# Kernel optimization log

Measured on AMD Instinct MI355X. Metric: run time of the kernel, lower is better.

Reference implementation:

```python
import jax, jax.numpy as jnp
import numpy as np

NUM_HEADS = 8


def setup_inputs() -> dict:
    key = jax.random.key(0)
    ks = jax.random.split(key, 8)
    B, N, H, W = 8, 1024, 32, 32
    dim = H * W  # 1024
    x1 = jax.random.normal(ks[0], (B, N, H, W), dtype=jnp.float32)
    x2 = jax.random.normal(ks[1], (B, N, H, W), dtype=jnp.float32)
    conv_w = jax.random.normal(ks[2], (N, 2 * N, 3, 3), dtype=jnp.float32) * 0.01
    conv_b = jnp.zeros((N,), dtype=jnp.float32)
    wq = jax.random.normal(ks[3], (dim, dim), dtype=jnp.float32) * 0.02
    wk = jax.random.normal(ks[4], (dim, dim), dtype=jnp.float32) * 0.02
    wv = jax.random.normal(ks[5], (dim, dim), dtype=jnp.float32) * 0.02
    proj_w = jax.random.normal(ks[6], (dim, dim), dtype=jnp.float32) * 0.02
    proj_b = jnp.zeros((dim,), dtype=jnp.float32)
    return {"x1": x1, "x2": x2, "conv_w": conv_w, "conv_b": conv_b,
            "wq": wq, "wk": wk, "wv": wv, "proj_w": proj_w, "proj_b": proj_b}


def reference(x1, x2, conv_w, conv_b, wq, wk, wv, proj_w, proj_b):
    B, N, H, W = x1.shape
    C = H * W
    nh = NUM_HEADS
    hd = C // nh
    scale = hd ** -0.5

    # conv_cat: Conv2d(2N -> N, k=3, pad=1) on channel-concatenated inputs
    x_cat = jnp.concatenate([x1, x2], axis=1)  # [B, 2N, H, W]
    x_cat = jax.lax.conv_general_dilated(
        x_cat, conv_w, window_strides=(1, 1), padding=((1, 1), (1, 1)),
        dimension_numbers=("NCHW", "OIHW", "NCHW"))
    x_cat = x_cat + conv_b[None, :, None, None]
    x_cat = x_cat.reshape(B, N, C)  # [B, N, C]

    # torch Linear: y = x @ W.T (no bias, qkv_bias=False)
    def heads(t):  # [B, N, C] -> [B, nh, N, hd]
        return t.reshape(B, N, nh, hd).transpose(0, 2, 1, 3)

    q = heads(x1.reshape(B, N, C) @ wq.T)
    k = heads(x_cat @ wk.T)
    v = heads(x_cat @ wv.T)

    # attention: softmax(q k^T * scale) v   (dropout is identity at p=0)
    attn = jnp.einsum("bhnd,bhmd->bhnm", q, k) * scale
    attn = jax.nn.softmax(attn, axis=-1)
    x_attn = jnp.einsum("bhnm,bhmd->bhnd", attn, v)  # [B, nh, N, hd]
    x_attn = x_attn.transpose(0, 2, 1, 3).reshape(B, N, C)

    out = (x_attn @ proj_w.T + proj_b).reshape(B, N, H, W) + x1
    return out
```

## Files before the change

### kernel.cpp

```cpp
#include <hip/hip_runtime.h>
#include <hip/hip_bf16.h>
#include <cstdint>
#include <cstddef>

typedef __attribute__((ext_vector_type(8))) short short8;
typedef __attribute__((ext_vector_type(4))) float f32x4;
typedef unsigned short u16;

static __device__ __forceinline__ u16 f2bf(float f) {
  __hip_bfloat16 h = __float2bfloat16(f);
  return *reinterpret_cast<u16*>(&h);
}

static __device__ __forceinline__ void gload16(const void* g, void* l) {
  __builtin_amdgcn_global_load_lds(
      (const __attribute__((address_space(1))) void*)g,
      (__attribute__((address_space(3))) void*)l, 16, 0, 0);
}


__global__ void cast4_k(const float* __restrict__ a, const float* __restrict__ b,
                        const float* __restrict__ c, const float* __restrict__ d,
                        u16* __restrict__ oa, u16* __restrict__ ob,
                        u16* __restrict__ oc, u16* __restrict__ od) {
  const int which = blockIdx.y;
  const float* src = (which == 0) ? a : (which == 1) ? b : (which == 2) ? c : d;
  u16* dst = (which == 0) ? oa : (which == 1) ? ob : (which == 2) ? oc : od;
  int i = blockIdx.x * 256 + threadIdx.x;
  float4 v = ((const float4*)src)[i];
  union { u16 u[4]; uint2 p; } r;
  r.u[0] = f2bf(v.x); r.u[1] = f2bf(v.y); r.u[2] = f2bf(v.z); r.u[3] = f2bf(v.w);
  ((uint2*)dst)[i] = r.p;
}

__global__ void build_pad(const float* __restrict__ x1, const float* __restrict__ x2,
                          u16* __restrict__ in_t_pad, u16* __restrict__ x1b) {
  __shared__ float tile[64][65];
  const int it = blockIdx.x;
  const int st = blockIdx.y;
  const int b  = blockIdx.z;
  const int i0 = it * 64, s0 = st * 64;
  const bool isx1 = (i0 < 1024);
  const float* src = isx1
      ? x1 + ((size_t)b * 1024 + i0) * 1024
      : x2 + ((size_t)b * 1024 + (i0 - 1024)) * 1024;
  const int t = threadIdx.x;
  #pragma unroll
  for (int jj = 0; jj < 16; ++jj) {
    int idx = jj * 256 + t;
    int ii = idx >> 6, si = idx & 63;
    float v = src[(size_t)ii * 1024 + s0 + si];
    tile[ii][si] = v;
    if (isx1)
      x1b[((size_t)b * 1024 + i0 + ii) * 1024 + s0 + si] = f2bf(v);
  }
  __syncthreads();
  #pragma unroll
  for (int jj = 0; jj < 16; ++jj) {
    int idx = jj * 256 + t;
    int si = idx >> 6, ii = idx & 63;
    const int s = s0 + si;
    const int prow = (b * 34 + (s >> 5) + 1) * 34 + (s & 31) + 1;
    in_t_pad[(size_t)prow * 2048 + i0 + ii] = f2bf(tile[ii][si]);
  }
}

__global__ void pack_wp(const float* __restrict__ cw, u16* __restrict__ Wp) {
  __shared__ float sb[2304];
  const int blk = blockIdx.x;
  const int t = threadIdx.x;
  const size_t base = (size_t)blk * 2304;
  #pragma unroll
  for (int jj = 0; jj < 9; ++jj) sb[jj * 256 + t] = cw[base + jj * 256 + t];
  __syncthreads();
  const int p = blk * 256 + t;
  #pragma unroll
  for (int q = 0; q < 9; ++q)
    Wp[(size_t)q * 2097152 + p] = f2bf(sb[t * 9 + q]);
}

__global__ void addc_k(const float* __restrict__ p, const float* __restrict__ bias,
                       u16* __restrict__ xc) {
  __shared__ float tile[64][65];
  const int st = blockIdx.x;
  const int ot = blockIdx.y;
  const int b  = blockIdx.z;
  const int s0 = st * 64, o0 = ot * 64;
  const int t = threadIdx.x;
  const float* p1 = p + 8388608;
  #pragma unroll
  for (int jj = 0; jj < 16; ++jj) {
    int idx = jj * 256 + t;
    int si = idx >> 6, oi = idx & 63;
    const size_t m = ((size_t)b * 1024 + s0 + si) * 1024 + o0 + oi;
    tile[si][oi] = p[m] + p1[m] + bias[o0 + oi];
  }
  __syncthreads();
  #pragma unroll
  for (int jj = 0; jj < 16; ++jj) {
    int idx = jj * 256 + t;
    int oi = idx >> 6, si = idx & 63;
    xc[((size_t)b * 1024 + o0 + oi) * 1024 + s0 + si] = f2bf(tile[si][oi]);
  }
}

enum { GM_PLAIN = 0, GM_PROJ = 2 };

__global__ __launch_bounds__(256, 1)
void conv9_k(const u16* __restrict__ Ap, const u16* __restrict__ B,
             float* __restrict__ Cf) {
  __shared__ u16 lds[2 * 12288 + 3 * 8192];
  const int tid = threadIdx.x;
  const int lane = tid & 63, w = tid >> 6;
  const int l15 = lane & 15, l4 = lane >> 4;

  const int bid = blockIdx.x;
  const int lb = (bid & 7) * 32 + (bid >> 3);
  const int kz = lb >> 7;
  const int tile = lb & 127;
  const int tm = tile >> 2, tn = tile & 3;
  const int row0 = tm * 256, col0 = tn * 256;
  const int b = tm >> 2;
  const int y0 = (tm & 3) * 8;
  const int hb = (b * 34 + y0) * 34;
  const int wr = (w >> 1) * 128, wc = (w & 1) * 128;
  const int chbase = kz * 1024;

  int pr[8];
  #pragma unroll
  for (int mi = 0; mi < 8; ++mi) {
    const int m = row0 + wr + mi * 16 + l15;
    const int y = (m >> 5) & 31, x = m & 31;
    pr[mi] = (y - y0 + 1) * 34 + x + 1;
  }

  const int srow = tid >> 2;
  const int sgc = tid & 3;

  f32x4 acc[8][8];
  #pragma unroll
  for (int i = 0; i < 8; ++i)
    #pragma unroll
    for (int jj = 0; jj < 8; ++jj)
      acc[i][jj] = (f32x4){0.f, 0.f, 0.f, 0.f};

  auto stageHalo = [&](int cc, int half) {
    u16* dst = lds + half * 12288;
    #pragma unroll
    for (int rnd = 0; rnd < 6; ++rnd) {
      const int row = rnd * 64 + srow;
      const int g = sgc ^ ((row >> 1) & 3);
      const u16* src = Ap + (size_t)(hb + row) * 2048 + chbase + cc * 32 + g * 8;
      gload16(src, dst + (size_t)(rnd * 256 + tid) * 8);
    }
  };
  auto stageB = [&](int cc, int q) {
    u16* dst = lds + 24576 + (q % 3) * 8192;
    #pragma unroll
    for (int rnd = 0; rnd < 4; ++rnd) {
      const int r = rnd * 64 + srow;
      const int g = sgc ^ ((r >> 1) & 3);
      const u16* src = B + ((size_t)q << 21) + (size_t)(col0 + r) * 2048
                       + chbase + cc * 32 + g * 8;
      gload16(src, dst + (size_t)(rnd * 256 + tid) * 8);
    }
  };

  constexpr int ddt[9] = {-35, -34, -33, -1, 0, 1, 33, 34, 35};
  constexpr int NC = 32;

  stageHalo(0, 0);
  stageHalo(1, 1);
  stageB(0, 0);
  stageB(0, 1);

  for (int cc = 0; cc < NC; ++cc) {
    const u16* hcur = lds + (cc & 1) * 12288;
    const bool interior = (cc >= 1 && cc <= NC - 2);
    #pragma unroll
    for (int q = 0; q < 9; ++q) {
      if ((q == 1 || q == 2) && interior) {
        asm volatile("s_waitcnt vmcnt(10)" ::: "memory");
      } else if (q == 8 && cc == NC - 1) {
        asm volatile("s_waitcnt vmcnt(0)" ::: "memory");
      } else {
        asm volatile("s_waitcnt vmcnt(4)" ::: "memory");
      }
      __builtin_amdgcn_s_barrier();
      {
        const int gp2 = cc * 9 + q + 2;
        if (gp2 <= NC * 9 - 1) {
          int qS = q + 2, ccS = cc;
          if (qS >= 9) { qS -= 9; ccS += 1; }
          stageB(ccS, qS);
        }
        if (q == 0 && cc >= 1 && cc <= NC - 2)
          stageHalo(cc + 1, (cc + 1) & 1);
      }
      {
        const u16* bq = lds + 24576 + (q % 3) * 8192;
        const int dd = ddt[q];
        short8 av[8], bv[8];
        #pragma unroll
        for (int mi = 0; mi < 8; ++mi) {
          const int hr = pr[mi] + dd;
          const int g = l4 ^ ((hr >> 1) & 3);
          av[mi] = *(const short8*)(hcur + hr * 32 + g * 8);
        }
        #pragma unroll
        for (int ni = 0; ni < 8; ++ni) {
          const int r = wc + ni * 16 + l15;
          const int g = l4 ^ ((r >> 1) & 3);
          bv[ni] = *(const short8*)(bq + r * 32 + g * 8);
        }
        __builtin_amdgcn_s_setprio(1);
        #pragma unroll
        for (int mi = 0; mi < 8; ++mi)
          #pragma unroll
          for (int ni = 0; ni < 8; ++ni)
            acc[mi][ni] = __builtin_amdgcn_mfma_f32_16x16x32_bf16(av[mi], bv[ni], acc[mi][ni], 0, 0, 0);
        __builtin_amdgcn_s_setprio(0);
      }
    }
  }

  #pragma unroll
  for (int mi = 0; mi < 8; ++mi) {
    #pragma unroll
    for (int ni = 0; ni < 8; ++ni) {
      #pragma unroll
      for (int j = 0; j < 4; ++j) {
        const int grow = row0 + wr + mi * 16 + l4 * 4 + j;
        const int gcol = col0 + wc + ni * 16 + l15;
        Cf[(size_t)kz * 8388608 + ((size_t)grow << 10) + gcol] = acc[mi][ni][j];
      }
    }
  }
}

template<int MODE>
__global__ __launch_bounds__(512, 2)
void gemm3_k(const u16* __restrict__ A, const u16* __restrict__ B,
             u16* __restrict__ Cb, float* __restrict__ Cf,
             const float* __restrict__ bias, const float* __restrict__ resid,
             int Ktot, int ntn_sh) {
  __shared__ u16 lds[3 * 24576];
  const int tid = threadIdx.x;
  const int lane = tid & 63;
  const int w = tid >> 6;
  const int l15 = lane & 15, l4 = lane >> 4;

  const int nwg = gridDim.x;
  const int bid = blockIdx.x;
  const int lb = (bid & 7) * (nwg >> 3) + (bid >> 3);
  const int tm = lb >> ntn_sh;
  const int tn = lb & ((1 << ntn_sh) - 1);
  const int row0 = tm * 256, col0 = tn * 128;
  const int wr = (w >> 1) * 64, wc = (w & 1) * 64;

  const int sr = w * 8 + (lane >> 3);
  const int pp = (lane & 7) ^ (lane >> 3);

  f32x4 acc[4][4];
  #pragma unroll
  for (int i = 0; i < 4; ++i)
    #pragma unroll
    for (int jj = 0; jj < 4; ++jj)
      acc[i][jj] = (f32x4){0.f, 0.f, 0.f, 0.f};

  const int nK = Ktot >> 6;

  auto stage = [&](int kt, u16* buf) {
    u16* da = buf + (size_t)w * 512;
    u16* db = buf + 16384 + (size_t)w * 512;
    const int k0 = kt << 6;
    #pragma unroll
    for (int u = 0; u < 4; ++u) {
      const u16* ga = A + (size_t)(row0 + u * 64 + sr) * Ktot + k0 + pp * 8;
      gload16(ga, da + u * 4096);
    }
    #pragma unroll
    for (int u = 0; u < 2; ++u) {
      const u16* gb = B + (size_t)(col0 + u * 64 + sr) * Ktot + k0 + pp * 8;
      gload16(gb, db + u * 4096);
    }
  };

  auto compute = [&](const u16* buf) {
    const char* Ar = (const char*)buf;
    const char* Br = (const char*)(buf + 16384);
    #pragma unroll
    for (int ks = 0; ks < 2; ++ks) {
      const int bcol = ((ks << 6) + (l4 << 4)) ^ ((l15 & 7) << 4);
      short8 av[4], bv[4];
      #pragma unroll
      for (int mi = 0; mi < 4; ++mi)
        av[mi] = *(const short8*)(Ar + (wr + mi * 16 + l15) * 128 + bcol);
      #pragma unroll
      for (int ni = 0; ni < 4; ++ni)
        bv[ni] = *(const short8*)(Br + (wc + ni * 16 + l15) * 128 + bcol);
      __builtin_amdgcn_s_setprio(1);
      #pragma unroll
      for (int mi = 0; mi < 4; ++mi)
        #pragma unroll
        for (int ni = 0; ni < 4; ++ni)
          acc[mi][ni] = __builtin_amdgcn_mfma_f32_16x16x32_bf16(av[mi], bv[ni], acc[mi][ni], 0, 0, 0);
      __builtin_amdgcn_s_setprio(0);
    }
  };

  u16* pb0 = lds;
  u16* pb1 = lds + 24576;
  u16* pb2 = lds + 49152;

  stage(0, pb0);
  stage(1, pb1);
  for (int t = 0; t < nK; ++t) {
    if (t + 1 < nK) {
      asm volatile("s_waitcnt vmcnt(6)" ::: "memory");
    } else {
      asm volatile("s_waitcnt vmcnt(0)" ::: "memory");
    }
    __builtin_amdgcn_s_barrier();
    if (t + 2 < nK) stage(t + 2, pb2);
    compute(pb0);
    u16* tmp = pb0; pb0 = pb1; pb1 = pb2; pb2 = tmp;
  }

  #pragma unroll
  for (int mi = 0; mi < 4; ++mi) {
    #pragma unroll
    for (int ni = 0; ni < 4; ++ni) {
      #pragma unroll
      for (int j = 0; j < 4; ++j) {
        const int grow = row0 + wr + mi * 16 + l4 * 4 + j;
        const int gcol = col0 + wc + ni * 16 + l15;
        const float v = acc[mi][ni][j];
        if constexpr (MODE == GM_PLAIN) {
          Cb[((size_t)grow << 10) + gcol] = f2bf(v);
        } else if constexpr (MODE == GM_PROJ) {
          const size_t o = ((size_t)grow << 10) + gcol;
          Cf[o] = v + bias[gcol] + resid[o];
        }
      }
    }
  }
}

__global__ __launch_bounds__(512, 4)
void qkv_k(const u16* __restrict__ Ax1, const u16* __restrict__ Axc,
           const u16* __restrict__ Wq, const u16* __restrict__ Wk,
           const u16* __restrict__ Wv,
           u16* __restrict__ Qb, u16* __restrict__ Kb, u16* __restrict__ Vtb) {
  __shared__ u16 lds[3 * 12288];
  const int tid = threadIdx.x;
  const int lane = tid & 63;
  const int w = tid >> 6;
  const int l15 = lane & 15, l4 = lane >> 4;

  const int bid = blockIdx.x;
  const int lb = (bid & 7) * 96 + (bid >> 3);
  const int sel = lb >> 8;
  const int sub = lb & 255;
  const int tm = sub >> 3, tn = sub & 7;
  const int row0 = tm * 256, col0 = tn * 128;
  const int wr = (w >> 1) * 64, wc = (w & 1) * 64;

  const u16* A = (sel == 0) ? Ax1 : Axc;
  const u16* B = (sel == 0) ? Wq : (sel == 1) ? Wk : Wv;

  const int str = tid >> 2;
  const int sgc = tid & 3;

  f32x4 acc[4][4];
  #pragma unroll
  for (int i = 0; i < 4; ++i)
    #pragma unroll
    for (int jj = 0; jj < 4; ++jj)
      acc[i][jj] = (f32x4){0.f, 0.f, 0.f, 0.f};

  constexpr int Ktot = 1024;
  const int nKt = Ktot >> 5;

  auto stage = [&](int kt, u16* buf) {
    const int k0 = kt << 5;
    #pragma unroll
    for (int u = 0; u < 2; ++u) {
      const int r = u * 128 + str;
      const int swz = sgc ^ ((r >> 1) & 3);
      const u16* ga = A + (size_t)(row0 + r) * Ktot + k0 + swz * 8;
      gload16(ga, buf + ((size_t)u * 512 + tid) * 8);
    }
    {
      const int swz = sgc ^ ((str >> 1) & 3);
      const u16* gb = B + (size_t)(col0 + str) * Ktot + k0 + swz * 8;
      gload16(gb, buf + 8192 + (size_t)tid * 8);
    }
  };

  auto compute = [&](const u16* buf) {
    short8 av[4], bv[4];
    #pragma unroll
    for (int mi = 0; mi < 4; ++mi) {
      const int row = wr + mi * 16 + l15;
      const int g = l4 ^ ((row >> 1) & 3);
      av[mi] = *(const short8*)(buf + row * 32 + g * 8);
    }
    #pragma unroll
    for (int ni = 0; ni < 4; ++ni) {
      const int row = wc + ni * 16 + l15;
      const int g = l4 ^ ((row >> 1) & 3);
      bv[ni] = *(const short8*)(buf + 8192 + row * 32 + g * 8);
    }
    __builtin_amdgcn_s_setprio(1);
    #pragma unroll
    for (int mi = 0; mi < 4; ++mi)
      #pragma unroll
      for (int ni = 0; ni < 4; ++ni)
        acc[mi][ni] = __builtin_amdgcn_mfma_f32_16x16x32_bf16(av[mi], bv[ni], acc[mi][ni], 0, 0, 0);
    __builtin_amdgcn_s_setprio(0);
  };

  u16* pb0 = lds;
  u16* pb1 = lds + 12288;
  u16* pb2 = lds + 24576;

  stage(0, pb0);
  stage(1, pb1);
  for (int t = 0; t < nKt; ++t) {
    if (t + 1 < nKt) {
      asm volatile("s_waitcnt vmcnt(3)" ::: "memory");
    } else {
      asm volatile("s_waitcnt vmcnt(0)" ::: "memory");
    }
    __builtin_amdgcn_s_barrier();
    if (t + 2 < nKt) stage(t + 2, pb2);
    compute(pb0);
    u16* tmp = pb0; pb0 = pb1; pb1 = pb2; pb2 = tmp;
  }

  if (sel < 2) {
    u16* Cb = (sel == 0) ? Qb : Kb;
    #pragma unroll
    for (int mi = 0; mi < 4; ++mi)
      #pragma unroll
      for (int ni = 0; ni < 4; ++ni)
        #pragma unroll
        for (int j = 0; j < 4; ++j) {
          const int grow = row0 + wr + mi * 16 + l4 * 4 + j;
          const int gcol = col0 + wc + ni * 16 + l15;
          Cb[((size_t)grow << 10) + gcol] = f2bf(acc[mi][ni][j]);
        }
  } else {
    const int h = tn;
    const int bb = row0 >> 10;
    u16* tb = lds;
    #pragma unroll
    for (int chunk = 0; chunk < 4; ++chunk) {
      __syncthreads();
      if ((w >> 1) == chunk) {
        #pragma unroll
        for (int mi = 0; mi < 4; ++mi)
          #pragma unroll
          for (int ni = 0; ni < 4; ++ni)
            #pragma unroll
            for (int j = 0; j < 4; ++j) {
              const int d = wc + ni * 16 + l15;
              const int t = mi * 16 + l4 * 4 + j;
              tb[d * 66 + t] = f2bf(acc[mi][ni][j]);
            }
      }
      __syncthreads();
      {
        const int r = tid >> 2;
        const int c0 = (tid & 3) * 16;
        const int tok = (row0 & 1023) + chunk * 64 + c0;
        uint4 v0 = *(const uint4*)(tb + r * 66 + c0);
        uint4 v1 = *(const uint4*)(tb + r * 66 + c0 + 8);
        u16* dst = Vtb + (((size_t)((bb * 8 + h) * 128 + r)) << 10) + tok;
        *(uint4*)dst = v0;
        *(uint4*)(dst + 8) = v1;
      }
    }
  }
}

__global__ __launch_bounds__(256, 2)
void attn2_k(const u16* __restrict__ Q, const u16* __restrict__ K,
             const u16* __restrict__ Vt, u16* __restrict__ O) {
  __shared__ u16 Ks[2][64 * 128];
  __shared__ u16 Vs[2][128 * 64];
  __shared__ u16 Plds[4][16 * 72];
  const int bid = blockIdx.x;
  const int lb = (bid & 7) * 128 + (bid >> 3);
  const int bh = lb >> 4;
  const int mtile = lb & 15;
  const int b = bh >> 3, h = bh & 7;
  const int tid = threadIdx.x, lane = tid & 63, w = tid >> 6;
  const int l15 = lane & 15, l4 = lane >> 4;

  short8 qf[4];
  {
    const int qrow = b * 1024 + mtile * 64 + w * 16 + l15;
    const u16* qb = Q + ((size_t)qrow << 10) + h * 128;
    #pragma unroll
    for (int kk = 0; kk < 4; ++kk)
      qf[kk] = *(const short8*)(qb + kk * 32 + l4 * 8);
  }

  f32x4 o[8];
  #pragma unroll
  for (int db = 0; db < 8; ++db) o[db] = (f32x4){0.f, 0.f, 0.f, 0.f};
  float mrow[4], lrow[4];
  #pragma unroll
  for (int j = 0; j < 4; ++j) { mrow[j] = -1e30f; lrow[j] = 0.f; }
  const float scale = 0.08838834764831845f;

  auto stageKV = [&](int kt, int half) {
    #pragma unroll
    for (int j = 0; j < 4; ++j) {
      const int c = (j * 4 + w) * 64 + lane;
      const int r = c >> 4;
      const int coff = (((c & 15) ^ (r & 7)) << 3);
      const u16* gp = K + ((size_t)(b * 1024 + kt * 64 + r) << 10) + h * 128 + coff;
      gload16(gp, (void*)(Ks[half] + (j * 4 + w) * 512));
    }
    #pragma unroll
    for (int j = 0; j < 4; ++j) {
      const int c = (j * 4 + w) * 64 + lane;
      const int r = c >> 3;
      const int coff = (((c & 7) ^ (r & 7)) << 3);
      const u16* gp = Vt + ((size_t)((b * 8 + h) * 128 + r) << 10) + kt * 64 + coff;
      gload16(gp, (void*)(Vs[half] + (j * 4 + w) * 512));
    }
  };

  stageKV(0, 0);
  for (int kt = 0; kt < 16; ++kt) {
    const int cur = kt & 1;
    asm volatile("s_waitcnt vmcnt(0)" ::: "memory");
    __builtin_amdgcn_s_barrier();
    if (kt + 1 < 16) stageKV(kt + 1, cur ^ 1);

    const u16* ks_ = Ks[cur];
    const u16* vs_ = Vs[cur];
    f32x4 s[4];
    #pragma unroll
    for (int cb = 0; cb < 4; ++cb) {
      s[cb] = (f32x4){0.f, 0.f, 0.f, 0.f};
      #pragma unroll
      for (int kk = 0; kk < 4; ++kk) {
        const int col = (kk * 32 + l4 * 8) ^ ((l15 & 7) << 3);
        short8 bK = *(const short8*)(ks_ + (cb * 16 + l15) * 128 + col);
        __builtin_amdgcn_s_setprio(1);
        s[cb] = __builtin_amdgcn_mfma_f32_16x16x32_bf16(qf[kk], bK, s[cb], 0, 0, 0);
        __builtin_amdgcn_s_setprio(0);
      }
    }
    #pragma unroll
    for (int cb = 0; cb < 4; ++cb) {
      s[cb][0] *= scale; s[cb][1] *= scale; s[cb][2] *= scale; s[cb][3] *= scale;
    }
    #pragma unroll
    for (int j = 0; j < 4; ++j) {
      float mx = fmaxf(fmaxf(s[0][j], s[1][j]), fmaxf(s[2][j], s[3][j]));
      #pragma unroll
      for (int off = 8; off >= 1; off >>= 1)
        mx = fmaxf(mx, __shfl_xor(mx, off, 64));
      const float mn = fmaxf(mrow[j], mx);
      const float fac = __expf(mrow[j] - mn);
      mrow[j] = mn;
      float rs = 0.f;
      #pragma unroll
      for (int cb = 0; cb < 4; ++cb) {
        const float p = __expf(s[cb][j] - mn);
        s[cb][j] = p;
        rs += p;
      }
      #pragma unroll
      for (int off = 8; off >= 1; off >>= 1)
        rs += __shfl_xor(rs, off, 64);
      lrow[j] = lrow[j] * fac + rs;
      #pragma unroll
      for (int db = 0; db < 8; ++db) o[db][j] *= fac;
    }
    u16* pl = Plds[w];
    #pragma unroll
    for (int cb = 0; cb < 4; ++cb)
      #pragma unroll
      for (int j = 0; j < 4; ++j)
        pl[(l4 * 4 + j) * 72 + cb * 16 + l15] = f2bf(s[cb][j]);
    asm volatile("s_waitcnt lgkmcnt(0)" ::: "memory");
    __builtin_amdgcn_sched_barrier(0);
    short8 ap[2];
    #pragma unroll
    for (int ks2 = 0; ks2 < 2; ++ks2)
      ap[ks2] = *(const short8*)(pl + l15 * 72 + ks2 * 32 + l4 * 8);
    #pragma unroll
    for (int db = 0; db < 8; ++db) {
      #pragma unroll
      for (int ks2 = 0; ks2 < 2; ++ks2) {
        const int col = (ks2 * 32 + l4 * 8) ^ ((l15 & 7) << 3);
        short8 bV = *(const short8*)(vs_ + (db * 16 + l15) * 64 + col);
        __builtin_amdgcn_s_setprio(1);
        o[db] = __builtin_amdgcn_mfma_f32_16x16x32_bf16(ap[ks2], bV, o[db], 0, 0, 0);
        __builtin_amdgcn_s_setprio(0);
      }
    }
  }
  #pragma unroll
  for (int db = 0; db < 8; ++db) {
    #pragma unroll
    for (int j = 0; j < 4; ++j) {
      const int grow = b * 1024 + mtile * 64 + w * 16 + l4 * 4 + j;
      const int gcol = h * 128 + db * 16 + l15;
      O[((size_t)grow << 10) + gcol] = f2bf(o[db][j] / lrow[j]);
    }
  }
}


extern "C" void kernel_launch(void* const* d_in, const int* in_sizes, int n_in,
                              void* d_out, int out_size, void* d_ws, size_t ws_size,
                              hipStream_t stream) {
  const float* x1     = (const float*)d_in[0];
  const float* x2     = (const float*)d_in[1];
  const float* conv_w = (const float*)d_in[2];
  const float* conv_b = (const float*)d_in[3];
  const float* wq     = (const float*)d_in[4];
  const float* wk     = (const float*)d_in[5];
  const float* wv     = (const float*)d_in[6];
  const float* proj_w = (const float*)d_in[7];
  const float* proj_b = (const float*)d_in[8];
  float* out = (float*)d_out;

  char* ws = (char*)d_ws;
  size_t off = 0;
  auto alloc = [&](size_t bytes) -> void* {
    void* p = ws + off;
    off += (bytes + 255) & ~(size_t)255;
    return p;
  };
  u16* x1b  = (u16*)alloc(8192ULL * 1024 * 2);
  u16* in_t_pad = (u16*)alloc((9248ULL + 96) * 2048 * 2);
  const size_t pad_bytes = 9248ULL * 2048 * 2;
  u16* Wp   = (u16*)alloc(9ULL * 2097152 * 2);
  u16* wqb  = (u16*)alloc(1048576ULL * 2);
  u16* wkb  = (u16*)alloc(1048576ULL * 2);
  u16* wvb  = (u16*)alloc(1048576ULL * 2);
  u16* pjb  = (u16*)alloc(1048576ULL * 2);
  u16* xc   = (u16*)alloc(8192ULL * 1024 * 2);
  u16* Qb   = (u16*)alloc(8192ULL * 1024 * 2);
  u16* Kb   = (u16*)alloc(8192ULL * 1024 * 2);
  u16* Vtb  = (u16*)alloc(8192ULL * 1024 * 2);
  u16* Ob   = (u16*)alloc(8192ULL * 1024 * 2);
  float* pConv = (float*)Qb;

  (void)hipMemsetAsync(in_t_pad, 0, pad_bytes + 96ULL * 2048 * 2, stream);
  cast4_k<<<dim3(1024, 4), 256, 0, stream>>>(wq, wk, wv, proj_w, wqb, wkb, wvb, pjb);
  build_pad<<<dim3(32, 16, 8), 256, 0, stream>>>(x1, x2, in_t_pad, x1b);
  pack_wp<<<8192, 256, 0, stream>>>(conv_w, Wp);

  conv9_k<<<256, 256, 0, stream>>>(in_t_pad, Wp, pConv);
  addc_k<<<dim3(16, 16, 8), 256, 0, stream>>>(pConv, conv_b, xc);
  qkv_k<<<768, 512, 0, stream>>>(x1b, xc, wqb, wkb, wvb, Qb, Kb, Vtb);
  attn2_k<<<1024, 256, 0, stream>>>(Qb, Kb, Vtb, Ob);
  gemm3_k<GM_PROJ><<<256, 512, 0, stream>>>(Ob, pjb, nullptr, out, proj_b, x1, 1024, 3);
}
```

Baseline: 497.5 us.

## Use 256x256-tile QKV GEMM and zero only the conv padding border

Replaces the QKV projection kernel with one that computes 256x256 output tiles, each split as 128x128 per wave, across 384 workgroups of 256 threads. The larger tiles raise data reuse per LDS load. The cost is a large register accumulator, one workgroup per CU and fewer resident waves to hide latency. It also replaces the full memset of the padded conv input buffer with a small kernel that zeroes only the spatial border pixels, since the interior is overwritten by build_pad. The extra tail rows of that buffer are no longer cleared.

Result: no change. 493.9 us (median of 3 runs) (-0.7%).

```diff
diff --git a/kernel.cpp b/kernel.cpp
--- a/kernel.cpp
+++ b/kernel.cpp
@@ -18,6 +18,17 @@
       (__attribute__((address_space(3))) void*)l, 16, 0, 0);
 }
 
+
+__global__ void border0_k(u16* __restrict__ in_t_pad) {
+  const int i = blockIdx.x;
+  const int b = blockIdx.y;
+  int py, px;
+  if (i < 34)      { py = 0;             px = i; }
+  else if (i < 68) { py = 33;            px = i - 34; }
+  else             { int j = i - 68;     py = 1 + (j >> 1); px = (j & 1) * 33; }
+  u16* dst = in_t_pad + ((size_t)((b * 34 + py) * 34 + px)) * 2048 + threadIdx.x * 8;
+  *(uint4*)dst = (uint4){0u, 0u, 0u, 0u};
+}
 
 __global__ void cast4_k(const float* __restrict__ a, const float* __restrict__ b,
                         const float* __restrict__ c, const float* __restrict__ d,
@@ -238,6 +249,156 @@
   }
 }
 
+__global__ __launch_bounds__(256, 1)
+void qkv2_k(const u16* __restrict__ x1b, const u16* __restrict__ xc,
+            const u16* __restrict__ wqb, const u16* __restrict__ wkb,
+            const u16* __restrict__ wvb,
+            u16* __restrict__ Qb, u16* __restrict__ Kb, u16* __restrict__ Vtb) {
+  __shared__ u16 lds[3 * 16384];
+  const int tid = threadIdx.x;
+  const int lane = tid & 63, w = tid >> 6;
+  const int l15 = lane & 15, l4 = lane >> 4;
+
+  const int bid = blockIdx.x;
+  const int lb = (bid & 7) * 48 + (bid >> 3);
+  int sel, tm, tn;
+  const u16 *A, *B;
+  if (lb < 128) {
+    sel = 0; tm = lb >> 2; tn = lb & 3;
+    A = x1b; B = wqb + (size_t)tn * 256 * 1024;
+  } else {
+    const int kv = lb - 128;
+    tm = kv >> 3; tn = kv & 7;
+    A = xc;
+    if (tn < 4) { sel = 1; B = wkb + (size_t)tn * 256 * 1024; }
+    else        { sel = 2; B = wvb + (size_t)(tn - 4) * 256 * 1024; }
+  }
+  const int row0 = tm * 256;
+  const int wr = (w >> 1) * 128, wc = (w & 1) * 128;
+
+  const int srow = tid >> 2;
+  const int sgc = tid & 3;
+
+  f32x4 acc[8][8];
+  #pragma unroll
+  for (int i = 0; i < 8; ++i)
+    #pragma unroll
+    for (int jj = 0; jj < 8; ++jj)
+      acc[i][jj] = (f32x4){0.f, 0.f, 0.f, 0.f};
+
+  auto stage = [&](int kt, u16* buf) {
+    const int k0 = kt << 5;
+    #pragma unroll
+    for (int u = 0; u < 4; ++u) {
+      const int r = u * 64 + srow;
+      const int g = sgc ^ ((r >> 1) & 3);
+      gload16(A + (size_t)(row0 + r) * 1024 + k0 + g * 8,
+              buf + (size_t)(u * 256 + tid) * 8);
+    }
+    #pragma unroll
+    for (int u = 0; u < 4; ++u) {
+      const int r = u * 64 + srow;
+      const int g = sgc ^ ((r >> 1) & 3);
+      gload16(B + (size_t)r * 1024 + k0 + g * 8,
+              buf + 8192 + (size_t)(u * 256 + tid) * 8);
+    }
+  };
+
+  auto compute = [&](const u16* buf) {
+    short8 av[8], bv[8];
+    #pragma unroll
+    for (int mi = 0; mi < 8; ++mi) {
+      const int r = wr + mi * 16 + l15;
+      const int g = l4 ^ ((r >> 1) & 3);
+      av[mi] = *(const short8*)(buf + r * 32 + g * 8);
+    }
+    #pragma unroll
+    for (int ni = 0; ni < 8; ++ni) {
+      const int r = wc + ni * 16 + l15;
+      const int g = l4 ^ ((r >> 1) & 3);
+      bv[ni] = *(const short8*)(buf + 8192 + r * 32 + g * 8);
+    }
+    __builtin_amdgcn_s_setprio(1);
+    #pragma unroll
+    for (int mi = 0; mi < 8; ++mi)
+      #pragma unroll
+      for (int ni = 0; ni < 8; ++ni)
+        acc[mi][ni] = __builtin_amdgcn_mfma_f32_16x16x32_bf16(av[mi], bv[ni], acc[mi][ni], 0, 0, 0);
+    __builtin_amdgcn_s_setprio(0);
+  };
+
+  u16* pb0 = lds;
+  u16* pb1 = lds + 16384;
+  u16* pb2 = lds + 32768;
+
+  stage(0, pb0);
+  stage(1, pb1);
+  for (int t = 0; t < 32; ++t) {
+    if (t + 1 < 32) {
+      asm volatile("s_waitcnt vmcnt(8)" ::: "memory");
+    } else {
+      asm volatile("s_waitcnt vmcnt(0)" ::: "memory");
+    }
+    __builtin_amdgcn_s_barrier();
+    if (t + 2 < 32) stage(t + 2, pb2);
+    compute(pb0);
+    u16* tmp = pb0; pb0 = pb1; pb1 = pb2; pb2 = tmp;
+  }
+
+  if (sel < 2) {
+    u16* out = (sel == 0) ? Qb : Kb;
+    const int colbase = tn * 256;
+    #pragma unroll
+    for (int mi = 0; mi < 8; ++mi)
+      #pragma unroll
+      for (int ni = 0; ni < 8; ++ni)
+        #pragma unroll
+        for (int j = 0; j < 4; ++j) {
+          const int grow = row0 + wr + mi * 16 + l4 * 4 + j;
+          const int gcol = colbase + wc + ni * 16 + l15;
+          out[((size_t)grow << 10) + gcol] = f2bf(acc[mi][ni][j]);
+        }
+  } else {
+    const int d0 = (tn - 4) * 256;
+    const int bb = row0 >> 10;
+    const int tok0 = row0 & 1023;
+    u16* tb = lds;
+    #pragma unroll
+    for (int c = 0; c < 4; ++c) {
+      __syncthreads();
+      if ((w >> 1) == (c >> 1)) {
+        const int mib = (c & 1) * 4;
+        #pragma unroll
+        for (int m2 = 0; m2 < 4; ++m2) {
+          const int mi = mib + m2;
+          #pragma unroll
+          for (int ni = 0; ni < 8; ++ni) {
+            const int d = wc + ni * 16 + l15;
+            #pragma unroll
+            for (int j = 0; j < 4; ++j) {
+              const int tl = mi * 16 + l4 * 4 + j - (c & 1) * 64;
+              tb[d * 66 + tl] = f2bf(acc[mi][ni][j]);
+            }
+          }
+        }
+      }
+      __syncthreads();
+      #pragma unroll
+      for (int p = 0; p < 4; ++p) {
+        const int dr = p * 64 + (tid >> 2);
+        const int t0 = (tid & 3) * 16;
+        uint4 v0 = *(const uint4*)(tb + dr * 66 + t0);
+        uint4 v1 = *(const uint4*)(tb + dr * 66 + t0 + 8);
+        const int dg = d0 + dr;
+        u16* dst = Vtb + (((size_t)((bb * 8 + (dg >> 7)) * 128 + (dg & 127))) << 10)
+                   + tok0 + c * 64 + t0;
+        *(uint4*)dst = v0;
+        *(uint4*)(dst + 8) = v1;
+      }
+    }
+  }
+}
+
 template<int MODE>
 __global__ __launch_bounds__(512, 2)
 void gemm3_k(const u16* __restrict__ A, const u16* __restrict__ B,
@@ -342,144 +503,6 @@
           const size_t o = ((size_t)grow << 10) + gcol;
           Cf[o] = v + bias[gcol] + resid[o];
         }
-      }
-    }
-  }
-}
-
-__global__ __launch_bounds__(512, 4)
-void qkv_k(const u16* __restrict__ Ax1, const u16* __restrict__ Axc,
-           const u16* __restrict__ Wq, const u16* __restrict__ Wk,
-           const u16* __restrict__ Wv,
-           u16* __restrict__ Qb, u16* __restrict__ Kb, u16* __restrict__ Vtb) {
-  __shared__ u16 lds[3 * 12288];
-  const int tid = threadIdx.x;
-  const int lane = tid & 63;
-  const int w = tid >> 6;
-  const int l15 = lane & 15, l4 = lane >> 4;
-
-  const int bid = blockIdx.x;
-  const int lb = (bid & 7) * 96 + (bid >> 3);
-  const int sel = lb >> 8;
-  const int sub = lb & 255;
-  const int tm = sub >> 3, tn = sub & 7;
-  const int row0 = tm * 256, col0 = tn * 128;
-  const int wr = (w >> 1) * 64, wc = (w & 1) * 64;
-
-  const u16* A = (sel == 0) ? Ax1 : Axc;
-  const u16* B = (sel == 0) ? Wq : (sel == 1) ? Wk : Wv;
-
-  const int str = tid >> 2;
-  const int sgc = tid & 3;
-
-  f32x4 acc[4][4];
-  #pragma unroll
-  for (int i = 0; i < 4; ++i)
-    #pragma unroll
-    for (int jj = 0; jj < 4; ++jj)
-      acc[i][jj] = (f32x4){0.f, 0.f, 0.f, 0.f};
-
-  constexpr int Ktot = 1024;
-  const int nKt = Ktot >> 5;
-
-  auto stage = [&](int kt, u16* buf) {
-    const int k0 = kt << 5;
-    #pragma unroll
-    for (int u = 0; u < 2; ++u) {
-      const int r = u * 128 + str;
-      const int swz = sgc ^ ((r >> 1) & 3);
-      const u16* ga = A + (size_t)(row0 + r) * Ktot + k0 + swz * 8;
-      gload16(ga, buf + ((size_t)u * 512 + tid) * 8);
-    }
-    {
-      const int swz = sgc ^ ((str >> 1) & 3);
-      const u16* gb = B + (size_t)(col0 + str) * Ktot + k0 + swz * 8;
-      gload16(gb, buf + 8192 + (size_t)tid * 8);
-    }
-  };
-
-  auto compute = [&](const u16* buf) {
-    short8 av[4], bv[4];
-    #pragma unroll
-    for (int mi = 0; mi < 4; ++mi) {
-      const int row = wr + mi * 16 + l15;
-      const int g = l4 ^ ((row >> 1) & 3);
-      av[mi] = *(const short8*)(buf + row * 32 + g * 8);
-    }
-    #pragma unroll
-    for (int ni = 0; ni < 4; ++ni) {
-      const int row = wc + ni * 16 + l15;
-      const int g = l4 ^ ((row >> 1) & 3);
-      bv[ni] = *(const short8*)(buf + 8192 + row * 32 + g * 8);
-    }
-    __builtin_amdgcn_s_setprio(1);
-    #pragma unroll
-    for (int mi = 0; mi < 4; ++mi)
-      #pragma unroll
-      for (int ni = 0; ni < 4; ++ni)
-        acc[mi][ni] = __builtin_amdgcn_mfma_f32_16x16x32_bf16(av[mi], bv[ni], acc[mi][ni], 0, 0, 0);
-    __builtin_amdgcn_s_setprio(0);
-  };
-
-  u16* pb0 = lds;
-  u16* pb1 = lds + 12288;
-  u16* pb2 = lds + 24576;
-
-  stage(0, pb0);
-  stage(1, pb1);
-  for (int t = 0; t < nKt; ++t) {
-    if (t + 1 < nKt) {
-      asm volatile("s_waitcnt vmcnt(3)" ::: "memory");
-    } else {
-      asm volatile("s_waitcnt vmcnt(0)" ::: "memory");
-    }
-    __builtin_amdgcn_s_barrier();
-    if (t + 2 < nKt) stage(t + 2, pb2);
-    compute(pb0);
-    u16* tmp = pb0; pb0 = pb1; pb1 = pb2; pb2 = tmp;
-  }
-
-  if (sel < 2) {
-    u16* Cb = (sel == 0) ? Qb : Kb;
-    #pragma unroll
-    for (int mi = 0; mi < 4; ++mi)
-      #pragma unroll
-      for (int ni = 0; ni < 4; ++ni)
-        #pragma unroll
-        for (int j = 0; j < 4; ++j) {
-          const int grow = row0 + wr + mi * 16 + l4 * 4 + j;
-          const int gcol = col0 + wc + ni * 16 + l15;
-          Cb[((size_t)grow << 10) + gcol] = f2bf(acc[mi][ni][j]);
-        }
-  } else {
-    const int h = tn;
-    const int bb = row0 >> 10;
-    u16* tb = lds;
-    #pragma unroll
-    for (int chunk = 0; chunk < 4; ++chunk) {
-      __syncthreads();
-      if ((w >> 1) == chunk) {
-        #pragma unroll
-        for (int mi = 0; mi < 4; ++mi)
-          #pragma unroll
-          for (int ni = 0; ni < 4; ++ni)
-            #pragma unroll
-            for (int j = 0; j < 4; ++j) {
-              const int d = wc + ni * 16 + l15;
-              const int t = mi * 16 + l4 * 4 + j;
-              tb[d * 66 + t] = f2bf(acc[mi][ni][j]);
-            }
-      }
-      __syncthreads();
-      {
-        const int r = tid >> 2;
-        const int c0 = (tid & 3) * 16;
-        const int tok = (row0 & 1023) + chunk * 64 + c0;
-        uint4 v0 = *(const uint4*)(tb + r * 66 + c0);
-        uint4 v1 = *(const uint4*)(tb + r * 66 + c0 + 8);
-        u16* dst = Vtb + (((size_t)((bb * 8 + h) * 128 + r)) << 10) + tok;
-        *(uint4*)dst = v0;
-        *(uint4*)(dst + 8) = v1;
       }
     }
   }
@@ -643,7 +666,6 @@
   };
   u16* x1b  = (u16*)alloc(8192ULL * 1024 * 2);
   u16* in_t_pad = (u16*)alloc((9248ULL + 96) * 2048 * 2);
-  const size_t pad_bytes = 9248ULL * 2048 * 2;
   u16* Wp   = (u16*)alloc(9ULL * 2097152 * 2);
   u16* wqb  = (u16*)alloc(1048576ULL * 2);
   u16* wkb  = (u16*)alloc(1048576ULL * 2);
@@ -656,14 +678,14 @@
   u16* Ob   = (u16*)alloc(8192ULL * 1024 * 2);
   float* pConv = (float*)Qb;
 
-  (void)hipMemsetAsync(in_t_pad, 0, pad_bytes + 96ULL * 2048 * 2, stream);
+  border0_k<<<dim3(132, 8), 256, 0, stream>>>(in_t_pad);
   cast4_k<<<dim3(1024, 4), 256, 0, stream>>>(wq, wk, wv, proj_w, wqb, wkb, wvb, pjb);
   build_pad<<<dim3(32, 16, 8), 256, 0, stream>>>(x1, x2, in_t_pad, x1b);
   pack_wp<<<8192, 256, 0, stream>>>(conv_w, Wp);
 
   conv9_k<<<256, 256, 0, stream>>>(in_t_pad, Wp, pConv);
   addc_k<<<dim3(16, 16, 8), 256, 0, stream>>>(pConv, conv_b, xc);
-  qkv_k<<<768, 512, 0, stream>>>(x1b, xc, wqb, wkb, wvb, Qb, Kb, Vtb);
+  qkv2_k<<<384, 256, 0, stream>>>(x1b, xc, wqb, wkb, wvb, Qb, Kb, Vtb);
   attn2_k<<<1024, 256, 0, stream>>>(Qb, Kb, Vtb, Ob);
   gemm3_k<GM_PROJ><<<256, 512, 0, stream>>>(Ob, pjb, nullptr, out, proj_b, x1, 1024, 3);
 }
```
